# Optimization experiments

Measured on AMD Instinct MI355X. Metric: run time of the kernel, lower is better.

The kernel has to match this reference:

```python
import jax, jax.numpy as jnp
import numpy as np

IN_DIM, OUT_DIM, EDGE_DIM = 128, 64, 16
BS, N = 8, 512

def setup_inputs() -> dict:
    key = jax.random.key(0)
    k1, k2, k3, k4 = jax.random.split(key, 4)
    x = jax.random.normal(k1, (BS, N, IN_DIM), dtype=jnp.float32)
    edge_feats = jax.random.normal(k2, (BS, N, N, EDGE_DIM), dtype=jnp.float32)
    # nn.Linear weights: fc (out_dim, in_dim), attn_fc (1, 2*out_dim+edge_dim)
    W_fc = jax.random.normal(k3, (OUT_DIM, IN_DIM), dtype=jnp.float32) / np.sqrt(IN_DIM)
    attn_w = jax.random.normal(k4, (2 * OUT_DIM + EDGE_DIM,), dtype=jnp.float32) / np.sqrt(2 * OUT_DIM + EDGE_DIM)
    return {"x": x, "edge_feats": edge_feats, "W_fc": W_fc, "attn_w": attn_w}

def reference(x, edge_feats, W_fc, attn_w):
    # h: (bs, N, out_dim)
    h = jnp.einsum('bni,oi->bno', x, W_fc)
    # Split attn_fc weight: concat([h_i, h_j, edge]) @ a == h_i@a_i + h_j@a_j + edge@a_e
    a_i = attn_w[:OUT_DIM]
    a_j = attn_w[OUT_DIM:2 * OUT_DIM]
    a_e = attn_w[2 * OUT_DIM:]
    s_i = jnp.einsum('bno,o->bn', h, a_i)              # (bs, N)
    s_j = jnp.einsum('bno,o->bn', h, a_j)              # (bs, N)
    s_e = jnp.einsum('bijk,k->bij', edge_feats, a_e)   # (bs, N, N)
    e_ij = s_i[:, :, None] + s_j[:, None, :] + s_e     # (bs, N, N)
    alpha = jax.nn.softmax(e_ij, axis=-1)              # softmax over j
    # weighted sum of h_j over j
    h_prime = jnp.einsum('bij,bjo->bio', alpha, h)
    return h_prime
```

## Files before the change

kernel.cpp:

```cpp
#include <hip/hip_runtime.h>

constexpr int IN_DIM = 128;
constexpr int OUT_DIM = 64;
constexpr int EDGE_DIM = 16;
constexpr int BS = 8;
constexpr int NN = 512;
constexpr int ROWS = BS * NN;
constexpr int TI = 4;

__global__ __launch_bounds__(256, 4) void fc_kernel(
    const float* __restrict__ x, const float* __restrict__ W,
    const float* __restrict__ attn_w,
    float* __restrict__ h, float* __restrict__ si, float* __restrict__ sj)
{
    __shared__ float xs[8 * IN_DIM];
    const int t    = threadIdx.x;
    const int lane = t & 63;
    const int w    = t >> 6;
    const int rowBase = blockIdx.x * 8;

    ((float4*)xs)[t] = ((const float4*)(x + (size_t)rowBase * IN_DIM))[t];

    const float a_i = attn_w[lane];
    const float a_j = attn_w[OUT_DIM + lane];
    __syncthreads();

    const float4* W4 = (const float4*)W;
    float acc0 = 0.f, acc1 = 0.f;
    const float4* xr0 = (const float4*)&xs[(w * 2 + 0) * IN_DIM];
    const float4* xr1 = (const float4*)&xs[(w * 2 + 1) * IN_DIM];
    #pragma unroll 8
    for (int k = 0; k < IN_DIM / 4; ++k) {
        const float4 wv = W4[lane * (IN_DIM / 4) + k];
        const float4 x0 = xr0[k];
        const float4 x1 = xr1[k];
        acc0 += x0.x * wv.x + x0.y * wv.y + x0.z * wv.z + x0.w * wv.w;
        acc1 += x1.x * wv.x + x1.y * wv.y + x1.z * wv.z + x1.w * wv.w;
    }
    #pragma unroll
    for (int r = 0; r < 2; ++r) {
        const float a   = r ? acc1 : acc0;
        const int   row = rowBase + w * 2 + r;
        h[(size_t)row * OUT_DIM + lane] = a;
        float pi = a * a_i;
        float pj = a * a_j;
        #pragma unroll
        for (int m = 32; m > 0; m >>= 1) {
            pi += __shfl_xor(pi, m, 64);
            pj += __shfl_xor(pj, m, 64);
        }
        if (lane == 0) { si[row] = pi; sj[row] = pj; }
    }
}

__global__ __launch_bounds__(256, 4) void attn_kernel(
    const float* __restrict__ edge, const float* __restrict__ attn_w,
    const float* __restrict__ h, const float* __restrict__ si,
    const float* __restrict__ sj, float* __restrict__ out)
{
    __shared__ float  alpha[TI * NN];
    __shared__ float4 part[TI][16][16];

    const int t    = threadIdx.x;
    const int lane = t & 63;
    const int w    = t >> 6;
    const int blk  = blockIdx.x;
    const int b    = blk >> 7;
    const int iRow = (blk & 127) * TI + w;
    const int rowg = (b << 9) + iRow;

    const float4* ae4 = (const float4*)(attn_w + 2 * OUT_DIM);
    const float4 ae0 = ae4[0], ae1 = ae4[1], ae2 = ae4[2], ae3 = ae4[3];
    const float  siv = si[rowg];
    const float4* ef4 = (const float4*)edge + (size_t)rowg * NN * EDGE_DIM / 4;
    const float* sjb  = sj + (b << 9);

    float e[8];
    #pragma unroll 2
    for (int jj = 0; jj < 8; ++jj) {
        const int j = jj * 64 + lane;
        const float4 v0 = ef4[j * 4 + 0], v1 = ef4[j * 4 + 1];
        const float4 v2 = ef4[j * 4 + 2], v3 = ef4[j * 4 + 3];
        const float se = v0.x * ae0.x + v0.y * ae0.y + v0.z * ae0.z + v0.w * ae0.w
                       + v1.x * ae1.x + v1.y * ae1.y + v1.z * ae1.z + v1.w * ae1.w
                       + v2.x * ae2.x + v2.y * ae2.y + v2.z * ae2.z + v2.w * ae2.w
                       + v3.x * ae3.x + v3.y * ae3.y + v3.z * ae3.z + v3.w * ae3.w;
        e[jj] = siv + sjb[j] + se;
    }

    float m = e[0];
    #pragma unroll
    for (int jj = 1; jj < 8; ++jj) m = fmaxf(m, e[jj]);
    #pragma unroll
    for (int msk = 32; msk > 0; msk >>= 1) m = fmaxf(m, __shfl_xor(m, msk, 64));

    float p[8], s = 0.f;
    #pragma unroll
    for (int jj = 0; jj < 8; ++jj) { p[jj] = __expf(e[jj] - m); s += p[jj]; }
    #pragma unroll
    for (int msk = 32; msk > 0; msk >>= 1) s += __shfl_xor(s, msk, 64);
    const float rinv = 1.0f / s;
    #pragma unroll
    for (int jj = 0; jj < 8; ++jj)
        alpha[w * NN + jj * 64 + lane] = p[jj] * rinv;

    __syncthreads();

    const int o4 = t & 15;
    const int g  = t >> 4;
    const float4* h4 = (const float4*)(h + ((size_t)(b << 9)) * OUT_DIM);
    float4 acc[TI];
    #pragma unroll
    for (int r = 0; r < TI; ++r) acc[r] = make_float4(0.f, 0.f, 0.f, 0.f);
    #pragma unroll 4
    for (int j = g; j < NN; j += 16) {
        const float4 hv = h4[j * 16 + o4];
        #pragma unroll
        for (int r = 0; r < TI; ++r) {
            const float a = alpha[r * NN + j];
            acc[r].x += a * hv.x; acc[r].y += a * hv.y;
            acc[r].z += a * hv.z; acc[r].w += a * hv.w;
        }
    }
    #pragma unroll
    for (int r = 0; r < TI; ++r) part[r][g][o4] = acc[r];
    __syncthreads();

    if (t < 64) {
        const int r = t >> 4, c = t & 15;
        float4 v = part[r][0][c];
        #pragma unroll
        for (int g2 = 1; g2 < 16; ++g2) {
            const float4 q = part[r][g2][c];
            v.x += q.x; v.y += q.y; v.z += q.z; v.w += q.w;
        }
        ((float4*)out)[((size_t)(b << 9) + (blk & 127) * TI + r) * 16 + c] = v;
    }
}

extern "C" void kernel_launch(void* const* d_in, const int* in_sizes, int n_in,
                              void* d_out, int out_size, void* d_ws, size_t ws_size,
                              hipStream_t stream) {
    const float* x      = (const float*)d_in[0];
    const float* edge   = (const float*)d_in[1];
    const float* W_fc   = (const float*)d_in[2];
    const float* attn_w = (const float*)d_in[3];
    float* out = (float*)d_out;

    float* h  = (float*)d_ws;
    float* si = h + (size_t)ROWS * OUT_DIM;
    float* sj = si + ROWS;

    fc_kernel<<<ROWS / 8, 256, 0, stream>>>(x, W_fc, attn_w, h, si, sj);
    attn_kernel<<<ROWS / TI, 256, 0, stream>>>(edge, attn_w, h, si, sj, out);
}
```

Baseline: 207.9 us.

## Fuse FC and attention into one cooperative kernel with coalesced edge loads

Merges the projection and attention kernels into a single cooperative launch. Grid-wide syncs separate the phases, and h is staged temporarily in the output buffer. The per-row s_i term is dropped because it cancels in the row softmax, and s_j is recomputed per block into shared memory. Edge features are now read with four lanes sharing each j as contiguous float4s, reduced with shuffles, which makes the dominant edge stream fully coalesced. In exchange, residency is capped at 512 blocks with two row tiles per block, which lowers occupancy for a bandwidth-bound stream and adds grid-sync overhead.

Measured after the change: 364.1 us. 1.75x slower.

```diff
diff --git a/kernel.cpp b/kernel.cpp
--- a/kernel.cpp
+++ b/kernel.cpp
@@ -1,140 +1,167 @@
 #include <hip/hip_runtime.h>
+#include <hip/hip_cooperative_groups.h>
 
-constexpr int IN_DIM = 128;
-constexpr int OUT_DIM = 64;
+namespace cg = cooperative_groups;
+
+constexpr int IN_DIM   = 128;
+constexpr int OUT_DIM  = 64;
 constexpr int EDGE_DIM = 16;
-constexpr int BS = 8;
-constexpr int NN = 512;
-constexpr int ROWS = BS * NN;
-constexpr int TI = 4;
+constexpr int BS       = 8;
+constexpr int NN       = 512;
+constexpr int ROWS     = BS * NN;
+constexpr int TI       = 4;
+constexpr int BLOCKS   = 512;
 
-__global__ __launch_bounds__(256, 4) void fc_kernel(
-    const float* __restrict__ x, const float* __restrict__ W,
-    const float* __restrict__ attn_w,
-    float* __restrict__ h, float* __restrict__ si, float* __restrict__ sj)
+struct SmemA {
+    float  xs[8 * IN_DIM];
+    float4 ws[64 * 33];
+};
+struct SmemB {
+    float  sjb[NN];
+    float  alpha[TI * NN];
+    float4 part[TI][16][16];
+};
+
+__global__ __launch_bounds__(256, 2) void gat_fused(
+    const float* __restrict__ x, const float* __restrict__ edge,
+    const float* __restrict__ W, const float* __restrict__ attn_w,
+    float* __restrict__ out)
 {
-    __shared__ float xs[8 * IN_DIM];
-    const int t    = threadIdx.x;
-    const int lane = t & 63;
-    const int w    = t >> 6;
-    const int rowBase = blockIdx.x * 8;
-
-    ((float4*)xs)[t] = ((const float4*)(x + (size_t)rowBase * IN_DIM))[t];
-
-    const float a_i = attn_w[lane];
-    const float a_j = attn_w[OUT_DIM + lane];
-    __syncthreads();
-
-    const float4* W4 = (const float4*)W;
-    float acc0 = 0.f, acc1 = 0.f;
-    const float4* xr0 = (const float4*)&xs[(w * 2 + 0) * IN_DIM];
-    const float4* xr1 = (const float4*)&xs[(w * 2 + 1) * IN_DIM];
-    #pragma unroll 8
-    for (int k = 0; k < IN_DIM / 4; ++k) {
-        const float4 wv = W4[lane * (IN_DIM / 4) + k];
-        const float4 x0 = xr0[k];
-        const float4 x1 = xr1[k];
-        acc0 += x0.x * wv.x + x0.y * wv.y + x0.z * wv.z + x0.w * wv.w;
-        acc1 += x1.x * wv.x + x1.y * wv.y + x1.z * wv.z + x1.w * wv.w;
-    }
-    #pragma unroll
-    for (int r = 0; r < 2; ++r) {
-        const float a   = r ? acc1 : acc0;
-        const int   row = rowBase + w * 2 + r;
-        h[(size_t)row * OUT_DIM + lane] = a;
-        float pi = a * a_i;
-        float pj = a * a_j;
-        #pragma unroll
-        for (int m = 32; m > 0; m >>= 1) {
-            pi += __shfl_xor(pi, m, 64);
-            pj += __shfl_xor(pj, m, 64);
-        }
-        if (lane == 0) { si[row] = pi; sj[row] = pj; }
-    }
-}
-
-__global__ __launch_bounds__(256, 4) void attn_kernel(
-    const float* __restrict__ edge, const float* __restrict__ attn_w,
-    const float* __restrict__ h, const float* __restrict__ si,
-    const float* __restrict__ sj, float* __restrict__ out)
-{
-    __shared__ float  alpha[TI * NN];
-    __shared__ float4 part[TI][16][16];
+    __shared__ union { SmemA a; SmemB b; } sm;
 
     const int t    = threadIdx.x;
     const int lane = t & 63;
     const int w    = t >> 6;
     const int blk  = blockIdx.x;
-    const int b    = blk >> 7;
-    const int iRow = (blk & 127) * TI + w;
-    const int rowg = (b << 9) + iRow;
+
+    {
+        const int rowBase = blk * 8;
+        ((float4*)sm.a.xs)[t] = ((const float4*)(x + (size_t)rowBase * IN_DIM))[t];
+        const float4* W4 = (const float4*)W;
+        #pragma unroll
+        for (int i = 0; i < 8; ++i) {
+            const int s = t + i * 256;
+            sm.a.ws[(s >> 5) * 33 + (s & 31)] = W4[s];
+        }
+        __syncthreads();
+        const float4* xr0 = (const float4*)&sm.a.xs[(w * 2 + 0) * IN_DIM];
+        const float4* xr1 = (const float4*)&sm.a.xs[(w * 2 + 1) * IN_DIM];
+        float acc0 = 0.f, acc1 = 0.f;
+        #pragma unroll 8
+        for (int k = 0; k < IN_DIM / 4; ++k) {
+            const float4 wv = sm.a.ws[lane * 33 + k];
+            const float4 x0 = xr0[k];
+            const float4 x1 = xr1[k];
+            acc0 += x0.x * wv.x + x0.y * wv.y + x0.z * wv.z + x0.w * wv.w;
+            acc1 += x1.x * wv.x + x1.y * wv.y + x1.z * wv.z + x1.w * wv.w;
+        }
+        out[(size_t)(rowBase + w * 2 + 0) * OUT_DIM + lane] = acc0;
+        out[(size_t)(rowBase + w * 2 + 1) * OUT_DIM + lane] = acc1;
+    }
+
+    cg::this_grid().sync();
+
+    const int b = blk >> 6;
+    const float4* h4 = (const float4*)(out + (((size_t)b) << 9) * OUT_DIM);
+    const int o4 = t & 15;
+    const int g  = t >> 4;
+
+    {
+        const float4 aj = ((const float4*)attn_w)[OUT_DIM / 4 + o4];
+        for (int it = 0; it < 32; ++it) {
+            const int j = it * 16 + g;
+            const float4 hv = h4[j * 16 + o4];
+            float p = hv.x * aj.x + hv.y * aj.y + hv.z * aj.z + hv.w * aj.w;
+            p += __shfl_xor(p, 1, 64);
+            p += __shfl_xor(p, 2, 64);
+            p += __shfl_xor(p, 4, 64);
+            p += __shfl_xor(p, 8, 64);
+            if (o4 == 0) sm.b.sjb[j] = p;
+        }
+    }
 
     const float4* ae4 = (const float4*)(attn_w + 2 * OUT_DIM);
-    const float4 ae0 = ae4[0], ae1 = ae4[1], ae2 = ae4[2], ae3 = ae4[3];
-    const float  siv = si[rowg];
-    const float4* ef4 = (const float4*)edge + (size_t)rowg * NN * EDGE_DIM / 4;
-    const float* sjb  = sj + (b << 9);
+    const float4 aesel = ae4[lane & 3];
+    float4 vt0 = make_float4(0.f, 0.f, 0.f, 0.f);
+    float4 vt1 = make_float4(0.f, 0.f, 0.f, 0.f);
 
-    float e[8];
-    #pragma unroll 2
-    for (int jj = 0; jj < 8; ++jj) {
-        const int j = jj * 64 + lane;
-        const float4 v0 = ef4[j * 4 + 0], v1 = ef4[j * 4 + 1];
-        const float4 v2 = ef4[j * 4 + 2], v3 = ef4[j * 4 + 3];
-        const float se = v0.x * ae0.x + v0.y * ae0.y + v0.z * ae0.z + v0.w * ae0.w
-                       + v1.x * ae1.x + v1.y * ae1.y + v1.z * ae1.z + v1.w * ae1.w
-                       + v2.x * ae2.x + v2.y * ae2.y + v2.z * ae2.z + v2.w * ae2.w
-                       + v3.x * ae3.x + v3.y * ae3.y + v3.z * ae3.z + v3.w * ae3.w;
-        e[jj] = siv + sjb[j] + se;
+    #pragma unroll
+    for (int tile = 0; tile < 2; ++tile) {
+        __syncthreads();
+
+        const int    iRow = ((blk & 63) * 2 + tile) * TI + w;
+        const size_t rowg = (((size_t)b) << 9) + iRow;
+        const float4* ef4 = (const float4*)edge + rowg * (NN * EDGE_DIM / 4);
+
+        float m = -1e30f;
+        #pragma unroll 4
+        for (int jj = 0; jj < 32; ++jj) {
+            const float4 v = ef4[jj * 64 + lane];
+            float pd = v.x * aesel.x + v.y * aesel.y + v.z * aesel.z + v.w * aesel.w;
+            pd += __shfl_xor(pd, 1, 64);
+            pd += __shfl_xor(pd, 2, 64);
+            const int jloc = jj * 16 + (lane >> 2);
+            const float ev = pd + sm.b.sjb[jloc];
+            m = fmaxf(m, ev);
+            if ((lane & 3) == 0) sm.b.alpha[w * NN + jloc] = ev;
+        }
+        #pragma unroll
+        for (int msk = 32; msk > 0; msk >>= 1) m = fmaxf(m, __shfl_xor(m, msk, 64));
+
+        float p[8], s = 0.f;
+        #pragma unroll
+        for (int jj = 0; jj < 8; ++jj) {
+            p[jj] = __expf(sm.b.alpha[w * NN + jj * 64 + lane] - m);
+            s += p[jj];
+        }
+        #pragma unroll
+        for (int msk = 32; msk > 0; msk >>= 1) s += __shfl_xor(s, msk, 64);
+        const float rinv = 1.0f / s;
+        #pragma unroll
+        for (int jj = 0; jj < 8; ++jj)
+            sm.b.alpha[w * NN + jj * 64 + lane] = p[jj] * rinv;
+
+        __syncthreads();
+
+        float4 acc[TI];
+        #pragma unroll
+        for (int r = 0; r < TI; ++r) acc[r] = make_float4(0.f, 0.f, 0.f, 0.f);
+        #pragma unroll 4
+        for (int j = g; j < NN; j += 16) {
+            const float4 hv = h4[j * 16 + o4];
+            #pragma unroll
+            for (int r = 0; r < TI; ++r) {
+                const float a = sm.b.alpha[r * NN + j];
+                acc[r].x += a * hv.x; acc[r].y += a * hv.y;
+                acc[r].z += a * hv.z; acc[r].w += a * hv.w;
+            }
+        }
+        #pragma unroll
+        for (int r = 0; r < TI; ++r) sm.b.part[r][g][o4] = acc[r];
+        __syncthreads();
+
+        float4 vv = make_float4(0.f, 0.f, 0.f, 0.f);
+        if (t < 64) {
+            const int r = t >> 4, c = t & 15;
+            vv = sm.b.part[r][0][c];
+            #pragma unroll
+            for (int g2 = 1; g2 < 16; ++g2) {
+                const float4 q = sm.b.part[r][g2][c];
+                vv.x += q.x; vv.y += q.y; vv.z += q.z; vv.w += q.w;
+            }
+        }
+        if (tile == 0) vt0 = vv; else vt1 = vv;
     }
 
-    float m = e[0];
-    #pragma unroll
-    for (int jj = 1; jj < 8; ++jj) m = fmaxf(m, e[jj]);
-    #pragma unroll
-    for (int msk = 32; msk > 0; msk >>= 1) m = fmaxf(m, __shfl_xor(m, msk, 64));
-
-    float p[8], s = 0.f;
-    #pragma unroll
-    for (int jj = 0; jj < 8; ++jj) { p[jj] = __expf(e[jj] - m); s += p[jj]; }
-    #pragma unroll
-    for (int msk = 32; msk > 0; msk >>= 1) s += __shfl_xor(s, msk, 64);
-    const float rinv = 1.0f / s;
-    #pragma unroll
-    for (int jj = 0; jj < 8; ++jj)
-        alpha[w * NN + jj * 64 + lane] = p[jj] * rinv;
-
-    __syncthreads();
-
-    const int o4 = t & 15;
-    const int g  = t >> 4;
-    const float4* h4 = (const float4*)(h + ((size_t)(b << 9)) * OUT_DIM);
-    float4 acc[TI];
-    #pragma unroll
-    for (int r = 0; r < TI; ++r) acc[r] = make_float4(0.f, 0.f, 0.f, 0.f);
-    #pragma unroll 4
-    for (int j = g; j < NN; j += 16) {
-        const float4 hv = h4[j * 16 + o4];
-        #pragma unroll
-        for (int r = 0; r < TI; ++r) {
-            const float a = alpha[r * NN + j];
-            acc[r].x += a * hv.x; acc[r].y += a * hv.y;
-            acc[r].z += a * hv.z; acc[r].w += a * hv.w;
-        }
-    }
-    #pragma unroll
-    for (int r = 0; r < TI; ++r) part[r][g][o4] = acc[r];
-    __syncthreads();
+    cg::this_grid().sync();
 
     if (t < 64) {
         const int r = t >> 4, c = t & 15;
-        float4 v = part[r][0][c];
-        #pragma unroll
-        for (int g2 = 1; g2 < 16; ++g2) {
-            const float4 q = part[r][g2][c];
-            v.x += q.x; v.y += q.y; v.z += q.z; v.w += q.w;
-        }
-        ((float4*)out)[((size_t)(b << 9) + (blk & 127) * TI + r) * 16 + c] = v;
+        const size_t obase = ((size_t)b) << 9;
+        const int i0 = ((blk & 63) * 2 + 0) * TI + r;
+        const int i1 = ((blk & 63) * 2 + 1) * TI + r;
+        ((float4*)out)[(obase + i0) * 16 + c] = vt0;
+        ((float4*)out)[(obase + i1) * 16 + c] = vt1;
     }
 }
 
@@ -147,10 +174,7 @@
     const float* attn_w = (const float*)d_in[3];
     float* out = (float*)d_out;
 
-    float* h  = (float*)d_ws;
-    float* si = h + (size_t)ROWS * OUT_DIM;
-    float* sj = si + ROWS;
-
-    fc_kernel<<<ROWS / 8, 256, 0, stream>>>(x, W_fc, attn_w, h, si, sj);
-    attn_kernel<<<ROWS / TI, 256, 0, stream>>>(edge, attn_w, h, si, sj, out);
+    void* args[] = { (void*)&x, (void*)&edge, (void*)&W_fc, (void*)&attn_w, (void*)&out };
+    hipLaunchCooperativeKernel((const void*)gat_fused, dim3(BLOCKS), dim3(256),
+                               args, 0, stream);
 }
```

## Drop softmax-invariant s_i term, stage W and s_j in LDS, parallelize final reduction

Applied to the files above, without the earlier changes.

Removes the per-row s_i computation and its use, since adding a constant per row does not change the softmax over j. In the FC kernel, W is staged in padded shared memory instead of being read from global memory inside the loop. In the attention kernel, s_j is staged in shared memory, the edge loop is unrolled further, and the final partial-sum reduction is spread across all four waves using shuffles instead of one wave doing a serial 16-way sum. Runtime is dominated by streaming the 128MB edge tensor, so these changes mostly trim overheads around that stream.

After: 205.1 us. Within noise of the previous version (-1.3%).

```diff
diff --git a/kernel.cpp b/kernel.cpp
--- a/kernel.cpp
+++ b/kernel.cpp
@@ -1,37 +1,41 @@
 #include <hip/hip_runtime.h>
 
-constexpr int IN_DIM = 128;
-constexpr int OUT_DIM = 64;
+constexpr int IN_DIM   = 128;
+constexpr int OUT_DIM  = 64;
 constexpr int EDGE_DIM = 16;
-constexpr int BS = 8;
-constexpr int NN = 512;
-constexpr int ROWS = BS * NN;
-constexpr int TI = 4;
+constexpr int BS       = 8;
+constexpr int NN       = 512;
+constexpr int ROWS     = BS * NN;
+constexpr int TI       = 4;
 
 __global__ __launch_bounds__(256, 4) void fc_kernel(
     const float* __restrict__ x, const float* __restrict__ W,
     const float* __restrict__ attn_w,
-    float* __restrict__ h, float* __restrict__ si, float* __restrict__ sj)
+    float* __restrict__ h, float* __restrict__ sj)
 {
-    __shared__ float xs[8 * IN_DIM];
+    __shared__ float  xs[8 * IN_DIM];
+    __shared__ float4 ws[64 * 33];
     const int t    = threadIdx.x;
     const int lane = t & 63;
     const int w    = t >> 6;
     const int rowBase = blockIdx.x * 8;
 
     ((float4*)xs)[t] = ((const float4*)(x + (size_t)rowBase * IN_DIM))[t];
-
-    const float a_i = attn_w[lane];
+    const float4* W4 = (const float4*)W;
+    #pragma unroll
+    for (int i = 0; i < 8; ++i) {
+        const int s = t + i * 256;
+        ws[(s >> 5) * 33 + (s & 31)] = W4[s];
+    }
     const float a_j = attn_w[OUT_DIM + lane];
     __syncthreads();
 
-    const float4* W4 = (const float4*)W;
-    float acc0 = 0.f, acc1 = 0.f;
     const float4* xr0 = (const float4*)&xs[(w * 2 + 0) * IN_DIM];
     const float4* xr1 = (const float4*)&xs[(w * 2 + 1) * IN_DIM];
+    float acc0 = 0.f, acc1 = 0.f;
     #pragma unroll 8
     for (int k = 0; k < IN_DIM / 4; ++k) {
-        const float4 wv = W4[lane * (IN_DIM / 4) + k];
+        const float4 wv = ws[lane * 33 + k];
         const float4 x0 = xr0[k];
         const float4 x1 = xr1[k];
         acc0 += x0.x * wv.x + x0.y * wv.y + x0.z * wv.z + x0.w * wv.w;
@@ -42,22 +46,19 @@
         const float a   = r ? acc1 : acc0;
         const int   row = rowBase + w * 2 + r;
         h[(size_t)row * OUT_DIM + lane] = a;
-        float pi = a * a_i;
         float pj = a * a_j;
         #pragma unroll
-        for (int m = 32; m > 0; m >>= 1) {
-            pi += __shfl_xor(pi, m, 64);
-            pj += __shfl_xor(pj, m, 64);
-        }
-        if (lane == 0) { si[row] = pi; sj[row] = pj; }
+        for (int m = 32; m > 0; m >>= 1) pj += __shfl_xor(pj, m, 64);
+        if (lane == 0) sj[row] = pj;
     }
 }
 
 __global__ __launch_bounds__(256, 4) void attn_kernel(
     const float* __restrict__ edge, const float* __restrict__ attn_w,
-    const float* __restrict__ h, const float* __restrict__ si,
-    const float* __restrict__ sj, float* __restrict__ out)
+    const float* __restrict__ h, const float* __restrict__ sj,
+    float* __restrict__ out)
 {
+    __shared__ float  sjb[NN];
     __shared__ float  alpha[TI * NN];
     __shared__ float4 part[TI][16][16];
 
@@ -67,16 +68,18 @@
     const int blk  = blockIdx.x;
     const int b    = blk >> 7;
     const int iRow = (blk & 127) * TI + w;
-    const int rowg = (b << 9) + iRow;
+    const size_t rowg = ((size_t)b << 9) + iRow;
+
+    if (t < 128)
+        ((float4*)sjb)[t] = ((const float4*)(sj + ((size_t)b << 9)))[t];
 
     const float4* ae4 = (const float4*)(attn_w + 2 * OUT_DIM);
     const float4 ae0 = ae4[0], ae1 = ae4[1], ae2 = ae4[2], ae3 = ae4[3];
-    const float  siv = si[rowg];
-    const float4* ef4 = (const float4*)edge + (size_t)rowg * NN * EDGE_DIM / 4;
-    const float* sjb  = sj + (b << 9);
+    const float4* ef4 = (const float4*)edge + rowg * (NN * EDGE_DIM / 4);
+    __syncthreads();
 
     float e[8];
-    #pragma unroll 2
+    #pragma unroll 4
     for (int jj = 0; jj < 8; ++jj) {
         const int j = jj * 64 + lane;
         const float4 v0 = ef4[j * 4 + 0], v1 = ef4[j * 4 + 1];
@@ -85,7 +88,7 @@
                        + v1.x * ae1.x + v1.y * ae1.y + v1.z * ae1.z + v1.w * ae1.w
                        + v2.x * ae2.x + v2.y * ae2.y + v2.z * ae2.z + v2.w * ae2.w
                        + v3.x * ae3.x + v3.y * ae3.y + v3.z * ae3.z + v3.w * ae3.w;
-        e[jj] = siv + sjb[j] + se;
+        e[jj] = sjb[j] + se;
     }
 
     float m = e[0];
@@ -108,7 +111,7 @@
 
     const int o4 = t & 15;
     const int g  = t >> 4;
-    const float4* h4 = (const float4*)(h + ((size_t)(b << 9)) * OUT_DIM);
+    const float4* h4 = (const float4*)(h + (((size_t)b) << 9) * OUT_DIM);
     float4 acc[TI];
     #pragma unroll
     for (int r = 0; r < TI; ++r) acc[r] = make_float4(0.f, 0.f, 0.f, 0.f);
@@ -126,15 +129,24 @@
     for (int r = 0; r < TI; ++r) part[r][g][o4] = acc[r];
     __syncthreads();
 
-    if (t < 64) {
-        const int r = t >> 4, c = t & 15;
-        float4 v = part[r][0][c];
+    {
+        const int c = lane & 15;
+        const int q = lane >> 4;
+        float4 v = part[w][q * 4 + 0][c];
         #pragma unroll
-        for (int g2 = 1; g2 < 16; ++g2) {
-            const float4 q = part[r][g2][c];
-            v.x += q.x; v.y += q.y; v.z += q.z; v.w += q.w;
+        for (int i = 1; i < 4; ++i) {
+            const float4 u = part[w][q * 4 + i][c];
+            v.x += u.x; v.y += u.y; v.z += u.z; v.w += u.w;
         }
-        ((float4*)out)[((size_t)(b << 9) + (blk & 127) * TI + r) * 16 + c] = v;
+        #pragma unroll
+        for (int msk = 16; msk <= 32; msk <<= 1) {
+            v.x += __shfl_xor(v.x, msk, 64);
+            v.y += __shfl_xor(v.y, msk, 64);
+            v.z += __shfl_xor(v.z, msk, 64);
+            v.w += __shfl_xor(v.w, msk, 64);
+        }
+        if (q == 0)
+            ((float4*)out)[rowg * 16 + c] = v;
     }
 }
 
@@ -148,9 +160,8 @@
     float* out = (float*)d_out;
 
     float* h  = (float*)d_ws;
-    float* si = h + (size_t)ROWS * OUT_DIM;
-    float* sj = si + ROWS;
+    float* sj = h + (size_t)ROWS * OUT_DIM;
 
-    fc_kernel<<<ROWS / 8, 256, 0, stream>>>(x, W_fc, attn_w, h, si, sj);
-    attn_kernel<<<ROWS / TI, 256, 0, stream>>>(edge, attn_w, h, si, sj, out);
+    fc_kernel<<<ROWS / 8, 256, 0, stream>>>(x, W_fc, attn_w, h, sj);
+    attn_kernel<<<ROWS / TI, 256, 0, stream>>>(edge, attn_w, h, sj, out);
 }
```
